# Kernel tuning notes

Measured on AMD Instinct MI355X. Metric: run time of the kernel, lower is better.

The kernel has to match this reference:

```python
import math
import jax, jax.numpy as jnp
from jax import lax
import numpy as np

NUM_EXPERTS = 8
TOP_K = 2
CAPACITY_FACTOR = 1.25
AUX_COEF = 0.01


def setup_inputs() -> dict:
    key = jax.random.key(0)
    k1, k2, k3, k4, k5 = jax.random.split(key, 5)
    B, T, C, I, E = 4, 2048, 768, 3072, NUM_EXPERTS
    x = jax.random.normal(k1, (B, T, C), dtype=jnp.float32)
    Wr = jax.random.normal(k2, (C, E), dtype=jnp.float32) * 0.02
    Wg = jax.random.normal(k3, (E, C, I), dtype=jnp.float32) * 0.02
    Wu = jax.random.normal(k4, (E, C, I), dtype=jnp.float32) * 0.02
    Wp = jax.random.normal(k5, (E, I, C), dtype=jnp.float32) * 0.02
    return {"x": x, "Wr": Wr, "Wg": Wg, "Wu": Wu, "Wp": Wp}


def reference(x, Wr, Wg, Wu, Wp):
    E, K = NUM_EXPERTS, TOP_K
    B, T, C = x.shape
    N = B * T
    capacity = max(1, math.ceil(CAPACITY_FACTOR * N / E))  # static: 1280
    xf = x.reshape(N, C)

    # --- router ---
    logits = xf @ Wr                                    # [N, E]
    probs = jax.nn.softmax(logits.astype(jnp.float32), axis=-1)
    gates, idx = lax.top_k(probs, K)                    # [N, 2] each
    gates = gates / jnp.clip(jnp.sum(gates, axis=-1, keepdims=True), 1e-9)

    # --- aux load-balancing loss ---
    oh1 = jax.nn.one_hot(idx[:, 0], E, dtype=jnp.int32)  # [N, E]
    oh2 = jax.nn.one_hot(idx[:, 1], E, dtype=jnp.int32)
    importance = probs.mean(axis=0)
    load = (oh1 + oh2).astype(jnp.float32).mean(axis=0) / K
    aux_loss = jnp.sum(importance * load) * E * AUX_COEF

    # --- capacity positions (running rank within each expert) ---
    pos1 = jnp.sum((jnp.cumsum(oh1, axis=0) - 1) * oh1, axis=-1)   # [N]
    mask1 = pos1 < capacity
    slot1 = idx[:, 0] * capacity + pos1
    count1 = jnp.minimum(jnp.sum(oh1, axis=0), capacity)           # [E]
    pos2 = jnp.sum((jnp.cumsum(oh2, axis=0) - 1) * oh2, axis=-1) + count1[idx[:, 1]]
    mask2 = pos2 < capacity
    slot2 = idx[:, 1] * capacity + pos2

    # --- dispatch (scatter into per-expert buffers; OOB slots dropped) ---
    buf = jnp.zeros((E * capacity, C), dtype=x.dtype)
    s1 = jnp.where(mask1, slot1, E * capacity)
    s2 = jnp.where(mask2, slot2, E * capacity)
    buf = buf.at[s1].set(xf, mode='drop')
    buf = buf.at[s2].set(xf, mode='drop')
    ein = buf.reshape(E, capacity, C)

    # --- per-expert swiglu MLP (grouped GEMMs) ---
    gate = jax.nn.silu(jnp.einsum('enc,ech->enh', ein, Wg))
    up = jnp.einsum('enc,ech->enh', ein, Wu)
    out = jnp.einsum('enh,ehc->enc', gate * up, Wp).reshape(E * capacity, C)

    # --- combine (gather back to token order, renormalized gates) ---
    g1 = gates[:, 0] * mask1.astype(jnp.float32)
    g2 = gates[:, 1] * mask2.astype(jnp.float32)
    denom = jnp.clip(g1 + g2, 1e-9)
    g1 = (g1 / denom).astype(x.dtype)
    g2 = (g2 / denom).astype(x.dtype)
    c1 = jnp.clip(slot1, 0, E * capacity - 1)
    c2 = jnp.clip(slot2, 0, E * capacity - 1)
    y = g1[:, None] * out[c1] + g2[:, None] * out[c2]
    return y.reshape(B, T, C), aux_loss
```

## Files before the change

### kernel.cpp

```cpp
#include <hip/hip_runtime.h>
#include <cstdint>
#include <cstddef>

#define NTOK 8192
#define NEXP 8
#define CAP 1280
#define CDIM 768
#define IDIM 3072
#define EROWS (NEXP*CAP)

typedef __attribute__((ext_vector_type(8))) short short8;
typedef __attribute__((ext_vector_type(4))) float f32x4;
typedef __attribute__((ext_vector_type(4))) unsigned short us4;

__device__ __forceinline__ unsigned short f2b(float f) {
  unsigned u = __builtin_bit_cast(unsigned, f);
  u += 0x7FFFu + ((u >> 16) & 1u);
  return (unsigned short)(u >> 16);
}

__global__ __launch_bounds__(256) void transpose_cvt(const float* __restrict__ src,
    unsigned short* __restrict__ dst, int R, int S) {
  int tilesS = S >> 5, tilesR = R >> 5;
  int perE = tilesR * tilesS;
  int e = blockIdx.x / perE;
  int rem = blockIdx.x % perE;
  int rt = rem / tilesS, st = rem % tilesS;
  const float* se = src + (size_t)e*R*S + ((size_t)rt*32)*S + st*32;
  unsigned short* de = dst + (size_t)e*R*S + ((size_t)st*32)*R + rt*32;
  __shared__ float tile[32][33];
  int tx = threadIdx.x & 31, ty = threadIdx.x >> 5;
#pragma unroll
  for (int k = 0; k < 4; ++k) tile[ty + 8*k][tx] = se[(size_t)(ty + 8*k)*S + tx];
  __syncthreads();
#pragma unroll
  for (int k = 0; k < 4; ++k) de[(size_t)(ty + 8*k)*R + tx] = f2b(tile[tx][ty + 8*k]);
}

__global__ __launch_bounds__(256) void router_kernel(const float* __restrict__ x,
    const float* __restrict__ Wr, float* __restrict__ probs,
    int* __restrict__ idx1, int* __restrict__ idx2,
    float* __restrict__ g1r, float* __restrict__ g2r) {
  __shared__ float WrT[NEXP*CDIM];
  for (int i = threadIdx.x; i < NEXP*CDIM; i += 256) {
    int c = i >> 3, e = i & 7;
    WrT[e*CDIM + c] = Wr[i];
  }
  __syncthreads();
  int w = threadIdx.x >> 6, l = threadIdx.x & 63;
  int t = blockIdx.x*4 + w;
  float acc[NEXP];
#pragma unroll
  for (int e = 0; e < NEXP; ++e) acc[e] = 0.f;
  for (int k = 0; k < CDIM/64; ++k) {
    float xv = x[(size_t)t*CDIM + k*64 + l];
#pragma unroll
    for (int e = 0; e < NEXP; ++e) acc[e] += xv * WrT[e*CDIM + k*64 + l];
  }
#pragma unroll
  for (int off = 32; off > 0; off >>= 1) {
#pragma unroll
    for (int e = 0; e < NEXP; ++e) acc[e] += __shfl_xor(acc[e], off);
  }
  if (l == 0) {
    float m = acc[0];
#pragma unroll
    for (int e = 1; e < NEXP; ++e) m = fmaxf(m, acc[e]);
    float p[NEXP]; float s = 0.f;
#pragma unroll
    for (int e = 0; e < NEXP; ++e) { p[e] = expf(acc[e] - m); s += p[e]; }
    float inv = 1.f / s;
#pragma unroll
    for (int e = 0; e < NEXP; ++e) { p[e] *= inv; probs[(size_t)t*NEXP + e] = p[e]; }
    int i1 = 0; float b1 = p[0];
#pragma unroll
    for (int e = 1; e < NEXP; ++e) if (p[e] > b1) { b1 = p[e]; i1 = e; }
    int i2 = -1; float b2 = -1e30f;
#pragma unroll
    for (int e = 0; e < NEXP; ++e) if (e != i1 && p[e] > b2) { b2 = p[e]; i2 = e; }
    float gs = fmaxf(b1 + b2, 1e-9f);
    g1r[t] = b1 / gs; g2r[t] = b2 / gs;
    idx1[t] = i1; idx2[t] = i2;
  }
}

__global__ __launch_bounds__(1024) void scan_kernel(
    const int* __restrict__ idx1, const int* __restrict__ idx2,
    const float* __restrict__ g1r, const float* __restrict__ g2r,
    const float* __restrict__ probs,
    int* __restrict__ bufmap,
    int* __restrict__ c1o, int* __restrict__ c2o,
    float* __restrict__ g1o, float* __restrict__ g2o,
    float* __restrict__ aux_out) {
  __shared__ unsigned int scanbuf[1024][9];
  __shared__ unsigned int totals[NEXP];
  int tid = threadIdx.x;
  int e1[8], e2[8];
  unsigned int cnt[NEXP];
#pragma unroll
  for (int k = 0; k < NEXP; ++k) cnt[k] = 0;
  for (int j = 0; j < 8; ++j) {
    int t = tid*8 + j;
    e1[j] = idx1[t]; e2[j] = idx2[t];
    cnt[e1[j]] += 1u;
    cnt[e2[j]] += (1u << 16);
  }
#pragma unroll
  for (int k = 0; k < NEXP; ++k) scanbuf[tid][k] = cnt[k];
  unsigned int run[NEXP];
#pragma unroll
  for (int k = 0; k < NEXP; ++k) run[k] = cnt[k];
  __syncthreads();
  for (int off = 1; off < 1024; off <<= 1) {
    unsigned int add[NEXP];
#pragma unroll
    for (int k = 0; k < NEXP; ++k) add[k] = 0;
    if (tid >= off) {
#pragma unroll
      for (int k = 0; k < NEXP; ++k) add[k] = scanbuf[tid - off][k];
    }
    __syncthreads();
#pragma unroll
    for (int k = 0; k < NEXP; ++k) { run[k] += add[k]; scanbuf[tid][k] = run[k]; }
    __syncthreads();
  }
  if (tid == 1023) {
#pragma unroll
    for (int k = 0; k < NEXP; ++k) totals[k] = run[k];
  }
  __syncthreads();
  unsigned int excl[NEXP];
#pragma unroll
  for (int k = 0; k < NEXP; ++k) excl[k] = run[k] - cnt[k];
  int cnt1c[NEXP];
#pragma unroll
  for (int k = 0; k < NEXP; ++k) cnt1c[k] = min((int)(totals[k] & 0xFFFFu), CAP);

  for (int j = 0; j < 8; ++j) {
    int t = tid*8 + j;
    int a = e1[j];
    int pos1 = (int)(excl[a] & 0xFFFFu); excl[a] += 1u;
    int slot1 = a*CAP + pos1;
    bool m1 = pos1 < CAP;
    if (m1) bufmap[slot1] = t;
    int b = e2[j];
    int pos2 = (int)(excl[b] >> 16) + cnt1c[b]; excl[b] += (1u << 16);
    int slot2 = b*CAP + pos2;
    bool m2 = pos2 < CAP;
    if (m2) bufmap[slot2] = t;
    float G1 = m1 ? g1r[t] : 0.f;
    float G2 = m2 ? g2r[t] : 0.f;
    float den = fmaxf(G1 + G2, 1e-9f);
    g1o[t] = G1 / den; g2o[t] = G2 / den;
    c1o[t] = min(slot1, EROWS - 1);
    c2o[t] = min(slot2, EROWS - 1);
  }

  float imp[NEXP];
#pragma unroll
  for (int k = 0; k < NEXP; ++k) imp[k] = 0.f;
  for (int j = 0; j < 8; ++j) {
    int t = tid*8 + j;
    const float4* pr = (const float4*)(probs + (size_t)t*NEXP);
    float4 a0 = pr[0], a1 = pr[1];
    imp[0] += a0.x; imp[1] += a0.y; imp[2] += a0.z; imp[3] += a0.w;
    imp[4] += a1.x; imp[5] += a1.y; imp[6] += a1.z; imp[7] += a1.w;
  }
  __syncthreads();
  float* fbuf = (float*)&scanbuf[0][0];
#pragma unroll
  for (int k = 0; k < NEXP; ++k) fbuf[tid*9 + k] = imp[k];
  __syncthreads();
  for (int s = 512; s >= 1; s >>= 1) {
    if (tid < s) {
#pragma unroll
      for (int k = 0; k < NEXP; ++k) fbuf[tid*9 + k] += fbuf[(tid + s)*9 + k];
    }
    __syncthreads();
  }
  if (tid == 0) {
    float aux = 0.f;
#pragma unroll
    for (int k = 0; k < NEXP; ++k) {
      float importance = fbuf[k] / (float)NTOK;
      float loadk = (float)((totals[k] & 0xFFFFu) + (totals[k] >> 16)) / ((float)NTOK * 2.0f);
      aux += importance * loadk;
    }
    aux_out[0] = aux * (float)NEXP * 0.01f;
  }
}

__global__ __launch_bounds__(192) void dispatch_kernel(const float* __restrict__ x,
    const int* __restrict__ bufmap, unsigned short* __restrict__ ein) {
  int r = blockIdx.x;
  int t = bufmap[r];
  int q = threadIdx.x;
  float4 v = make_float4(0.f, 0.f, 0.f, 0.f);
  if (t >= 0) v = ((const float4*)x)[(size_t)t*(CDIM/4) + q];
  us4 o;
  o.x = f2b(v.x); o.y = f2b(v.y); o.z = f2b(v.z); o.w = f2b(v.w);
  ((us4*)ein)[(size_t)r*(CDIM/4) + q] = o;
}

template<int K, bool DUAL, bool NOUTER>
__global__ __launch_bounds__(256, 2) void gemm_bt(
    const unsigned short* __restrict__ A,
    const unsigned short* __restrict__ B0,
    const unsigned short* __restrict__ B1,
    unsigned short* __restrict__ Hout,
    float* __restrict__ Fout,
    int Ntiles, int N) {
  constexpr int MT = 10;
  int chunk = gridDim.x >> 3;
  int bid = blockIdx.x;
  int tile = (bid & 7)*chunk + (bid >> 3);
  int perE = MT * Ntiles;
  int e = tile / perE, rem = tile % perE;
  int mt, nt;
  if (NOUTER) { nt = rem / MT; mt = rem % MT; }
  else        { mt = rem / Ntiles; nt = rem % Ntiles; }

  const unsigned short* Ae  = A  + (size_t)e*CAP*K + (size_t)mt*128*K;
  const unsigned short* B0e = B0 + (size_t)e*N*K   + (size_t)nt*128*K;
  const unsigned short* B1e = nullptr;
  if constexpr (DUAL) B1e = B1 + (size_t)e*N*K + (size_t)nt*128*K;

  __shared__ unsigned short Alds[128*64];
  __shared__ unsigned short B0lds[128*64];
  __shared__ unsigned short B1lds[DUAL ? 128*64 : 8];

  int tid = threadIdx.x;
  int l = tid & 63, w = tid >> 6;
  int rbase = w*8 + (l >> 3);
  int csrc  = (l & 7) ^ ((l >> 3) & 7);
  size_t gbase = (size_t)rbase*K + (size_t)csrc*8;
  int ldsoff = w*512;

  f32x4 acc0[16];
  f32x4 acc1[DUAL ? 16 : 1];
#pragma unroll
  for (int i = 0; i < 16; ++i) acc0[i] = (f32x4){0.f,0.f,0.f,0.f};
  if constexpr (DUAL) {
#pragma unroll
    for (int i = 0; i < 16; ++i) acc1[i] = (f32x4){0.f,0.f,0.f,0.f};
  }

  int wm = (w >> 1)*64, wn = (w & 1)*64;
  int lrow = l & 15, khi = l >> 4;

  for (int kt = 0; kt < K/64; ++kt) {
    const unsigned short* Ag  = Ae  + gbase + (size_t)kt*64;
    const unsigned short* Bg0 = B0e + gbase + (size_t)kt*64;
#pragma unroll
    for (int q = 0; q < 4; ++q) {
      __builtin_amdgcn_global_load_lds(
          (const __attribute__((address_space(1))) void*)(Ag + (size_t)q*32*K),
          (__attribute__((address_space(3))) void*)(Alds + ldsoff + q*2048), 16, 0, 0);
    }
#pragma unroll
    for (int q = 0; q < 4; ++q) {
      __builtin_amdgcn_global_load_lds(
          (const __attribute__((address_space(1))) void*)(Bg0 + (size_t)q*32*K),
          (__attribute__((address_space(3))) void*)(B0lds + ldsoff + q*2048), 16, 0, 0);
    }
    if constexpr (DUAL) {
      const unsigned short* Bg1 = B1e + gbase + (size_t)kt*64;
#pragma unroll
      for (int q = 0; q < 4; ++q) {
        __builtin_amdgcn_global_load_lds(
            (const __attribute__((address_space(1))) void*)(Bg1 + (size_t)q*32*K),
            (__attribute__((address_space(3))) void*)(B1lds + ldsoff + q*2048), 16, 0, 0);
      }
    }
    __syncthreads();
#pragma unroll
    for (int kk = 0; kk < 2; ++kk) {
      int cs = (kk*4 + khi) ^ (l & 7);
      short8 af[4];
#pragma unroll
      for (int m = 0; m < 4; ++m) {
        int row = wm + m*16 + lrow;
        af[m] = *(const short8*)(Alds + row*64 + cs*8);
      }
#pragma unroll
      for (int n = 0; n < 4; ++n) {
        int rowb = wn + n*16 + lrow;
        short8 b0 = *(const short8*)(B0lds + rowb*64 + cs*8);
#pragma unroll
        for (int m = 0; m < 4; ++m)
          acc0[m*4+n] = __builtin_amdgcn_mfma_f32_16x16x32_bf16(af[m], b0, acc0[m*4+n], 0, 0, 0);
        if constexpr (DUAL) {
          short8 b1 = *(const short8*)(B1lds + rowb*64 + cs*8);
#pragma unroll
          for (int m = 0; m < 4; ++m)
            acc1[m*4+n] = __builtin_amdgcn_mfma_f32_16x16x32_bf16(af[m], b1, acc1[m*4+n], 0, 0, 0);
        }
      }
    }
    __syncthreads();
  }

  if constexpr (DUAL) {
    unsigned short* Hp = Hout + (size_t)e*CAP*N + (size_t)mt*128*N + (size_t)nt*128;
#pragma unroll
    for (int m = 0; m < 4; ++m) {
#pragma unroll
      for (int n = 0; n < 4; ++n) {
        f32x4 g = acc0[m*4+n], u = acc1[m*4+n];
#pragma unroll
        for (int r = 0; r < 4; ++r) {
          int row = wm + m*16 + khi*4 + r;
          int col = wn + n*16 + lrow;
          float gv = g[r];
          float hv = gv / (1.f + __expf(-gv)) * u[r];
          Hp[(size_t)row*N + col] = f2b(hv);
        }
      }
    }
  } else {
    float* Fp = Fout + (size_t)e*CAP*N + (size_t)mt*128*N + (size_t)nt*128;
#pragma unroll
    for (int m = 0; m < 4; ++m) {
#pragma unroll
      for (int n = 0; n < 4; ++n) {
        f32x4 v = acc0[m*4+n];
#pragma unroll
        for (int r = 0; r < 4; ++r) {
          int row = wm + m*16 + khi*4 + r;
          int col = wn + n*16 + lrow;
          Fp[(size_t)row*N + col] = v[r];
        }
      }
    }
  }
}

__global__ __launch_bounds__(192) void combine_kernel(const float* __restrict__ outbuf,
    const int* __restrict__ c1, const int* __restrict__ c2,
    const float* __restrict__ g1, const float* __restrict__ g2,
    float* __restrict__ y) {
  int t = blockIdx.x;
  int q = threadIdx.x;
  float f1 = g1[t], f2 = g2[t];
  int a = c1[t], b = c2[t];
  float4 va = ((const float4*)outbuf)[(size_t)a*(CDIM/4) + q];
  float4 vb = ((const float4*)outbuf)[(size_t)b*(CDIM/4) + q];
  float4 r;
  r.x = f1*va.x + f2*vb.x;
  r.y = f1*va.y + f2*vb.y;
  r.z = f1*va.z + f2*vb.z;
  r.w = f1*va.w + f2*vb.w;
  ((float4*)y)[(size_t)t*(CDIM/4) + q] = r;
}

extern "C" void kernel_launch(void* const* d_in, const int* in_sizes, int n_in,
                              void* d_out, int out_size, void* d_ws, size_t ws_size,
                              hipStream_t stream) {
  const float* x  = (const float*)d_in[0];
  const float* Wr = (const float*)d_in[1];
  const float* Wg = (const float*)d_in[2];
  const float* Wu = (const float*)d_in[3];
  const float* Wp = (const float*)d_in[4];
  float* y = (float*)d_out;

  char* p = (char*)d_ws;
  auto alloc = [&](size_t bytes) { char* r = p; p += (bytes + 255) & ~(size_t)255; return r; };
  unsigned short* WgT = (unsigned short*)alloc((size_t)NEXP*IDIM*CDIM*2);
  unsigned short* WuT = (unsigned short*)alloc((size_t)NEXP*IDIM*CDIM*2);
  unsigned short* WpT = (unsigned short*)alloc((size_t)NEXP*CDIM*IDIM*2);
  unsigned short* ein = (unsigned short*)alloc((size_t)EROWS*CDIM*2);
  unsigned short* h   = (unsigned short*)alloc((size_t)EROWS*IDIM*2);
  float* outbuf = (float*)alloc((size_t)EROWS*CDIM*4);
  float* probs  = (float*)alloc((size_t)NTOK*NEXP*4);
  int* idx1 = (int*)alloc(NTOK*4);
  int* idx2 = (int*)alloc(NTOK*4);
  int* c1   = (int*)alloc(NTOK*4);
  int* c2   = (int*)alloc(NTOK*4);
  float* g1r = (float*)alloc(NTOK*4);
  float* g2r = (float*)alloc(NTOK*4);
  float* g1o = (float*)alloc(NTOK*4);
  float* g2o = (float*)alloc(NTOK*4);
  int* bufmap = (int*)alloc(EROWS*4);

  size_t required = (size_t)(p - (char*)d_ws);
  if (ws_size < required) return;

  hipMemsetAsync(bufmap, 0xFF, EROWS*sizeof(int), stream);

  transpose_cvt<<<NEXP*(CDIM/32)*(IDIM/32), 256, 0, stream>>>(Wg, WgT, CDIM, IDIM);
  transpose_cvt<<<NEXP*(CDIM/32)*(IDIM/32), 256, 0, stream>>>(Wu, WuT, CDIM, IDIM);
  transpose_cvt<<<NEXP*(IDIM/32)*(CDIM/32), 256, 0, stream>>>(Wp, WpT, IDIM, CDIM);

  router_kernel<<<NTOK/4, 256, 0, stream>>>(x, Wr, probs, idx1, idx2, g1r, g2r);
  scan_kernel<<<1, 1024, 0, stream>>>(idx1, idx2, g1r, g2r, probs, bufmap,
                                      c1, c2, g1o, g2o, y + (size_t)NTOK*CDIM);
  dispatch_kernel<<<EROWS, 192, 0, stream>>>(x, bufmap, ein);

  gemm_bt<CDIM, true, true><<<NEXP*10*(IDIM/128), 256, 0, stream>>>(
      ein, WgT, WuT, h, nullptr, IDIM/128, IDIM);
  gemm_bt<IDIM, false, false><<<NEXP*10*(CDIM/128), 256, 0, stream>>>(
      h, WpT, nullptr, nullptr, outbuf, CDIM/128, CDIM);

  combine_kernel<<<NTOK, 192, 0, stream>>>(outbuf, c1, c2, g1o, g2o, y);
}
```

Measured before the change: 327.5 us.

## Replace gate/up GEMM with interleaved-weight 256x256 eight-phase pipelined kernel

Fuses the Wg and Wu transpose/convert into one kernel that writes an interleaved weight layout, with gate and up rows alternating in 16-row groups. That layout lets a single GEMM produce matching gate and up accumulators for the SwiGLU epilogue. The new 512-thread GEMM uses 256x256 tiles, direct global-to-LDS loads with XOR swizzle, double-buffered LDS and an eight-phase schedule of barriers and setprio around the MFMA groups, so loads overlap compute. It aims to raise MFMA utilization in the first expert GEMM, at the cost of heavy register and LDS use and hand-tuned wait counts.

```diff
diff --git a/kernel.cpp b/kernel.cpp
--- a/kernel.cpp
+++ b/kernel.cpp
@@ -35,6 +35,29 @@
   __syncthreads();
 #pragma unroll
   for (int k = 0; k < 4; ++k) de[(size_t)(ty + 8*k)*R + tx] = f2b(tile[tx][ty + 8*k]);
+}
+
+__global__ __launch_bounds__(256) void wgu_cvt(const float* __restrict__ Wg,
+    const float* __restrict__ Wu, unsigned short* __restrict__ Wgu) {
+  const int tilesR = CDIM/32, tilesS = IDIM/32;
+  const int perE = tilesR * tilesS;
+  int sel = blockIdx.x / (NEXP*perE);
+  int rem = blockIdx.x % (NEXP*perE);
+  int e = rem / perE; int r2 = rem % perE;
+  int rt = r2 / tilesS, st = r2 % tilesS;
+  const float* src = (sel ? Wu : Wg) + (size_t)e*CDIM*IDIM + ((size_t)rt*32)*IDIM + st*32;
+  __shared__ float tile[32][33];
+  int tx = threadIdx.x & 31, ty = threadIdx.x >> 5;
+#pragma unroll
+  for (int k = 0; k < 4; ++k) tile[ty + 8*k][tx] = src[(size_t)(ty + 8*k)*IDIM + tx];
+  __syncthreads();
+  unsigned short* dstE = Wgu + (size_t)e*(2*IDIM)*CDIM;
+#pragma unroll
+  for (int k = 0; k < 4; ++k) {
+    int i = st*32 + ty + 8*k;
+    int np = 32*(i>>4) + (i&15) + sel*16;
+    dstE[(size_t)np*CDIM + rt*32 + tx] = f2b(tile[tx][ty + 8*k]);
+  }
 }
 
 __global__ __launch_bounds__(256) void router_kernel(const float* __restrict__ x,
@@ -202,6 +225,125 @@
   ((us4*)ein)[(size_t)r*(CDIM/4) + q] = o;
 }
 
+#define BAR  asm volatile("s_barrier" ::: "memory")
+#define VMW(N) asm volatile("s_waitcnt vmcnt(" #N ")" ::: "memory")
+#define P1 __builtin_amdgcn_s_setprio(1)
+#define P0 __builtin_amdgcn_s_setprio(0)
+
+template<int KD>
+__global__ __launch_bounds__(512, 2) void gemm1_8ph(
+    const unsigned short* __restrict__ A,
+    const unsigned short* __restrict__ Bw,
+    unsigned short* __restrict__ H) {
+  constexpr int NT = KD/64;
+  constexpr int NITER = NT/2;
+  __shared__ unsigned short lds[65536];
+
+  const int bid = blockIdx.x;
+  const int chunk = gridDim.x >> 3;
+  const int tile = (bid & 7)*chunk + (bid >> 3);
+  const int e = tile / 120;
+  const int rem = tile % 120;
+  const int nt = rem / 5, mt = rem % 5;
+
+  const int tid = threadIdx.x;
+  const int l = tid & 63, wid = tid >> 6;
+  const int wr = wid >> 2, wc = wid & 3;
+  const int lrow = l & 15, khi = l >> 4;
+
+  const unsigned short* Ab = A  + (size_t)e*CAP*KD    + (size_t)mt*256*KD;
+  const unsigned short* Bb = Bw + (size_t)e*(2*IDIM)*KD + (size_t)nt*256*KD;
+
+  const int srow = tid >> 3;
+  const int scol = (tid & 7) ^ (srow & 7);
+  const size_t lane_off = (size_t)srow*KD + scol*8;
+  const int lds_st = wid*512;
+
+#define STG(buf, op, half, kt) do { \
+    const unsigned short* s_ = ((op) ? Bb : Ab) + lane_off + (size_t)(half)*128*KD + (size_t)(kt)*64; \
+    unsigned short* d_ = (unsigned short*)lds + (buf)*32768 + (op)*16384 + (half)*8192 + lds_st; \
+    __builtin_amdgcn_global_load_lds((const __attribute__((address_space(1))) void*)s_, \
+        (__attribute__((address_space(3))) void*)d_, 16, 0, 0); \
+    __builtin_amdgcn_global_load_lds((const __attribute__((address_space(1))) void*)(s_ + (size_t)64*KD), \
+        (__attribute__((address_space(3))) void*)(d_ + 4096), 16, 0, 0); \
+  } while(0)
+
+  const int swz0 = ((khi    ) ^ (lrow & 7)) * 8;
+  const int swz1 = ((4 + khi) ^ (lrow & 7)) * 8;
+  const int abase = wr*8192 + lrow*64;
+  const int bbase = 16384 + (wc>>1)*8192 + ((wc&1)*64 + lrow)*64;
+
+#define LDA(buf, dst, mb) do { _Pragma("unroll") for (int m_=0;m_<4;++m_) { \
+    dst[m_][0] = *(const short8*)(lds + (buf)*32768 + abase + ((mb)+m_)*1024 + swz0); \
+    dst[m_][1] = *(const short8*)(lds + (buf)*32768 + abase + ((mb)+m_)*1024 + swz1); } } while(0)
+#define LDB(buf, dst, nb) do { _Pragma("unroll") for (int n_=0;n_<2;++n_) { \
+    dst[n_][0] = *(const short8*)(lds + (buf)*32768 + bbase + ((nb)+n_)*1024 + swz0); \
+    dst[n_][1] = *(const short8*)(lds + (buf)*32768 + bbase + ((nb)+n_)*1024 + swz1); } } while(0)
+#define QUAD(af, bf, mb, nb) do { _Pragma("unroll") for (int n_=0;n_<2;++n_) \
+    _Pragma("unroll") for (int m_=0;m_<4;++m_) { \
+      acc[(mb)+m_][(nb)+n_] = __builtin_amdgcn_mfma_f32_16x16x32_bf16(af[m_][0], bf[n_][0], acc[(mb)+m_][(nb)+n_], 0,0,0); \
+      acc[(mb)+m_][(nb)+n_] = __builtin_amdgcn_mfma_f32_16x16x32_bf16(af[m_][1], bf[n_][1], acc[(mb)+m_][(nb)+n_], 0,0,0); } } while(0)
+
+  f32x4 acc[8][4];
+#pragma unroll
+  for (int i = 0; i < 8; ++i)
+#pragma unroll
+    for (int j = 0; j < 4; ++j) acc[i][j] = (f32x4){0.f,0.f,0.f,0.f};
+
+  short8 a[4][2], bl[2][2], bh[2][2];
+
+  STG(0,0,0,0); STG(0,0,1,0); STG(0,1,0,0); STG(0,1,1,0);
+  STG(1,1,0,1); STG(1,1,1,1); STG(1,0,0,1);
+  VMW(6);
+  BAR;
+
+#define ITER(tY, t2, t3, DOS2, VM4, VM8) \
+    LDA(0,a,0); LDB(0,bl,0); STG(1,0,1,(tY)); \
+    BAR; P1; QUAD(a,bl,0,0); P0; BAR; \
+    LDB(0,bh,2); \
+    BAR; P1; QUAD(a,bh,0,2); P0; BAR; \
+    LDA(0,a,4); if (DOS2) STG(0,1,0,(t2)); \
+    BAR; P1; QUAD(a,bh,4,2); P0; BAR; \
+    if (DOS2) STG(0,1,1,(t2)); VM4; \
+    BAR; P1; QUAD(a,bl,4,0); P0; BAR; \
+    LDA(1,a,0); LDB(1,bl,0); if (DOS2) STG(0,0,0,(t2)); \
+    BAR; P1; QUAD(a,bl,0,0); P0; BAR; \
+    LDB(1,bh,2); if (DOS2) STG(0,0,1,(t2)); \
+    BAR; P1; QUAD(a,bh,0,2); P0; BAR; \
+    LDA(1,a,4); if (DOS2) STG(1,1,0,(t3)); \
+    BAR; P1; QUAD(a,bh,4,2); P0; BAR; \
+    if (DOS2) { STG(1,1,1,(t3)); STG(1,0,0,(t3)); } VM8; \
+    BAR; P1; QUAD(a,bl,4,0); P0; BAR;
+
+#pragma unroll 1
+  for (int i = 0; i < NITER-1; ++i) {
+    const int tY = 2*i+1, t2 = 2*i+2, t3 = 2*i+3;
+    ITER(tY, t2, t3, true, VMW(4), VMW(6));
+  }
+  ITER(NT-1, 0, 0, false, VMW(0), VMW(0));
+
+#undef ITER
+#undef QUAD
+#undef LDB
+#undef LDA
+#undef STG
+
+  const size_t rb = (size_t)e*CAP + (size_t)mt*256 + wr*128 + khi*4;
+  const size_t cb = (size_t)nt*128 + wc*32 + lrow;
+#pragma unroll
+  for (int m = 0; m < 8; ++m)
+#pragma unroll
+    for (int p = 0; p < 2; ++p) {
+      f32x4 g = acc[m][2*p], u = acc[m][2*p+1];
+#pragma unroll
+      for (int r = 0; r < 4; ++r) {
+        float gv = g[r];
+        float hv = gv / (1.f + __expf(-gv)) * u[r];
+        H[(rb + m*16 + r)*(size_t)IDIM + cb + p*16] = f2b(hv);
+      }
+    }
+}
+
 template<int K, bool DUAL, bool NOUTER>
 __global__ __launch_bounds__(256, 2) void gemm_bt(
     const unsigned short* __restrict__ A,
@@ -365,11 +507,10 @@
 
   char* p = (char*)d_ws;
   auto alloc = [&](size_t bytes) { char* r = p; p += (bytes + 255) & ~(size_t)255; return r; };
-  unsigned short* WgT = (unsigned short*)alloc((size_t)NEXP*IDIM*CDIM*2);
-  unsigned short* WuT = (unsigned short*)alloc((size_t)NEXP*IDIM*CDIM*2);
-  unsigned short* WpT = (unsigned short*)alloc((size_t)NEXP*CDIM*IDIM*2);
-  unsigned short* ein = (unsigned short*)alloc((size_t)EROWS*CDIM*2);
-  unsigned short* h   = (unsigned short*)alloc((size_t)EROWS*IDIM*2);
+  unsigned short* WguT = (unsigned short*)alloc((size_t)NEXP*2*IDIM*CDIM*2);
+  unsigned short* WpT  = (unsigned short*)alloc((size_t)NEXP*CDIM*IDIM*2);
+  unsigned short* ein  = (unsigned short*)alloc((size_t)EROWS*CDIM*2);
+  unsigned short* h    = (unsigned short*)alloc((size_t)EROWS*IDIM*2);
   float* outbuf = (float*)alloc((size_t)EROWS*CDIM*4);
   float* probs  = (float*)alloc((size_t)NTOK*NEXP*4);
   int* idx1 = (int*)alloc(NTOK*4);
@@ -387,8 +528,7 @@
 
   hipMemsetAsync(bufmap, 0xFF, EROWS*sizeof(int), stream);
 
-  transpose_cvt<<<NEXP*(CDIM/32)*(IDIM/32), 256, 0, stream>>>(Wg, WgT, CDIM, IDIM);
-  transpose_cvt<<<NEXP*(CDIM/32)*(IDIM/32), 256, 0, stream>>>(Wu, WuT, CDIM, IDIM);
+  wgu_cvt<<<2*NEXP*(CDIM/32)*(IDIM/32), 256, 0, stream>>>(Wg, Wu, WguT);
   transpose_cvt<<<NEXP*(IDIM/32)*(CDIM/32), 256, 0, stream>>>(Wp, WpT, IDIM, CDIM);
 
   router_kernel<<<NTOK/4, 256, 0, stream>>>(x, Wr, probs, idx1, idx2, g1r, g2r);
@@ -396,8 +536,7 @@
                                       c1, c2, g1o, g2o, y + (size_t)NTOK*CDIM);
   dispatch_kernel<<<EROWS, 192, 0, stream>>>(x, bufmap, ein);
 
-  gemm_bt<CDIM, true, true><<<NEXP*10*(IDIM/128), 256, 0, stream>>>(
-      ein, WgT, WuT, h, nullptr, IDIM/128, IDIM);
+  gemm1_8ph<CDIM><<<NEXP*5*(2*IDIM/256), 512, 0, stream>>>(ein, WguT, h);
   gemm_bt<IDIM, false, false><<<NEXP*10*(CDIM/128), 256, 0, stream>>>(
       h, WpT, nullptr, nullptr, outbuf, CDIM/128, CDIM);
 
```

Result: faster. 317.1 us (-3.2%).
